# Kernel optimization log

Measured on AMD Instinct MI355X. Metric: run time of the kernel, lower is better.

## Reference

```python
import jax, jax.numpy as jnp
import numpy as np

OFFS = [(dy, dx) for dy in (-1, 0, 1) for dx in (-1, 0, 1)]  # ME centered 3x3 region


def _build_maps():
    """Build the sparse coordinate pyramid and per-offset kernel maps, exactly
    mirroring MinkowskiEngine: out coords of a stride-2 conv are unique(c//2),
    and a pair (i_in, i_out) exists iff coord_out*stride + offset is active."""
    G = 1024
    rng = np.random.default_rng(0)
    flat = np.sort(rng.choice(G * G, size=300000, replace=False))
    coords = [np.stack(np.unravel_index(flat, (G, G)), axis=1).astype(np.int64)]
    grids = [G]
    for _ in range(3):
        coords.append(np.unique(coords[-1] // 2, axis=0))
        grids.append(grids[-1] // 2)

    def lut(c, g):
        t = -np.ones(g * g, np.int64)
        t[c[:, 0] * g + c[:, 1]] = np.arange(len(c))
        return t

    luts = [lut(c, g) for c, g in zip(coords, grids)]

    def kmap(lvl_in, c_out, stride):
        g, L = grids[lvl_in], luts[lvl_in]
        n_in, n_out = len(coords[lvl_in]), len(c_out)
        base = c_out * stride
        pairs = []
        for dy, dx in OFFS:
            q = base + np.array([dy, dx])
            ok = (q[:, 0] >= 0) & (q[:, 0] < g) & (q[:, 1] >= 0) & (q[:, 1] < g)
            key = np.clip(q[:, 0] * g + q[:, 1], 0, g * g - 1)
            idx = np.where(ok, L[key], -1)
            sel = np.nonzero(idx >= 0)[0]
            pairs.append((idx[sel], sel))
        M = max(len(p[0]) for p in pairs)
        ii = np.full((9, M), n_in, np.int32)   # pad -> dummy zero input row
        oo = np.full((9, M), n_out, np.int32)  # pad -> dummy output row (dropped)
        for k, (a, b) in enumerate(pairs):
            ii[k, :len(a)] = a
            oo[k, :len(b)] = b
        return ii, oo

    maps = {
        'c0': kmap(0, coords[0], 1), 'd0': kmap(0, coords[1], 2),
        'c1': kmap(1, coords[1], 1), 'd1': kmap(1, coords[2], 2),
        'c2': kmap(2, coords[2], 1), 'd2': kmap(2, coords[3], 2),
    }
    return maps, [len(c) for c in coords]


def setup_inputs() -> dict:
    maps, (n0, n1, n2, n3) = _build_maps()
    ks = jax.random.split(jax.random.key(0), 16)
    d = {'feats': jax.random.normal(ks[0], (n0, 1), jnp.float32)}
    chans = [(1, 64), (64, 128), (128, 128), (128, 128), (128, 128), (128, 128)]
    names = ['c0', 'd0', 'c1', 'd1', 'c2', 'd2']
    for i, (nm, (ci, co)) in enumerate(zip(names, chans)):
        d[f'w_{nm}'] = jax.random.normal(ks[1 + 2 * i], (9, ci, co), jnp.float32) / np.sqrt(9.0 * ci)
        d[f'b_{nm}'] = jax.random.normal(ks[2 + 2 * i], (co,), jnp.float32) * 0.01
        d[f'in_{nm}'] = jnp.asarray(maps[nm][0])
        d[f'out_{nm}'] = jnp.asarray(maps[nm][1])
    d.update(n0=n0, n1=n1, n2=n2, n3=n3)
    return d


def sparse_conv(feats, w, b, in_idx, out_idx, n_out):
    """Gather-GEMM-scatter sparse conv. w: [9, Cin, Cout]. Padded pairs point at a
    dummy zero input row (index n_in) and a dummy output row (index n_out)."""
    n_in, cin = feats.shape
    fp = jnp.concatenate([feats, jnp.zeros((1, cin), feats.dtype)], axis=0)
    out = jnp.zeros((n_out + 1, w.shape[2]), feats.dtype)
    for k in range(9):  # fixed kernel volume
        out = out.at[out_idx[k]].add(fp[in_idx[k]] @ w[k])
    return out[:n_out] + b


def reference(feats, w_c0, b_c0, in_c0, out_c0, w_d0, b_d0, in_d0, out_d0,
              w_c1, b_c1, in_c1, out_c1, w_d1, b_d1, in_d1, out_d1,
              w_c2, b_c2, in_c2, out_c2, w_d2, b_d2, in_d2, out_d2,
              n0, n1, n2, n3):
    x = sparse_conv(feats, w_c0, b_c0, in_c0, out_c0, n0)
    out0 = jax.nn.relu(sparse_conv(x, w_d0, b_d0, in_d0, out_d0, n1))
    y = sparse_conv(out0, w_c1, b_c1, in_c1, out_c1, n1)
    out1 = jax.nn.relu(sparse_conv(y, w_d1, b_d1, in_d1, out_d1, n2))
    z = sparse_conv(out1, w_c2, b_c2, in_c2, out_c2, n2)
    out2 = sparse_conv(z, w_d2, b_d2, in_d2, out_d2, n3)
    return (out2, out1, out0)
```

## Files before the change

kernel.cpp:

```cpp
#include <hip/hip_runtime.h>
#include <stdint.h>
#include <algorithm>


#define DI __device__ __forceinline__

typedef __attribute__((ext_vector_type(8))) short bf16x8;
typedef __attribute__((ext_vector_type(4))) float f32x4;

DI uint16_t f2bf(float x){
  union{float f;uint32_t i;}v; v.f=x;
  uint32_t r = v.i + 0x7fffu + ((v.i>>16)&1u);
  return (uint16_t)(r>>16);
}
DI uint32_t pack2(float a, float b){
  return (uint32_t)f2bf(a) | ((uint32_t)f2bf(b) << 16);
}
DI void gload16(const void* g, void* l){
  __builtin_amdgcn_global_load_lds(
      (const __attribute__((address_space(1))) void*)g,
      (__attribute__((address_space(3))) void*)l, 16, 0, 0);
}

__global__ __launch_bounds__(256) void diag_kernel(float* __restrict__ out, long n, float c){
  long i = (long)blockIdx.x*256 + threadIdx.x;
  if (i < n) out[i] = c;
}

__global__ __launch_bounds__(256) void init_all_kernel(
    int* __restrict__ tab, long ntab, float* __restrict__ zp){
  long i = (long)blockIdx.x*256 + threadIdx.x;
  if (i < ntab) tab[i] = -1;
  if (blockIdx.x == 0 && threadIdx.x < 64) zp[threadIdx.x] = 0.f;
}

struct BuildArgs {
  const int* im[6];
  const int* om[6];
  int   M[6];
  int   nin[6];
  int   nout[6];
  long  toff[6];
};

__global__ __launch_bounds__(256) void build_all_kernel(
    BuildArgs a, int* __restrict__ tb){
  const int L = blockIdx.z, k = blockIdx.y;
  const int M = a.M[L];
  long t = (long)blockIdx.x*256 + threadIdx.x;
  if (t >= M) return;
  int ii = a.im[L][(long)k*M + t];
  int oo = a.om[L][(long)k*M + t];
  if (ii >= 0 && ii < a.nin[L] && oo >= 0 && oo < a.nout[L])
    tb[a.toff[L] + (long)k*a.nout[L] + oo] = ii;
}

__global__ __launch_bounds__(256) void prep_all_kernel(
    const float* __restrict__ w0, const float* __restrict__ w1,
    const float* __restrict__ w2, const float* __restrict__ w3,
    const float* __restrict__ w4, uint16_t* __restrict__ wb, long total){
  const long wt64 = 9L*128*64, wt128 = 9L*128*128;
  long idx = (long)blockIdx.x*256 + threadIdx.x;
  if (idx >= total) return;
  int L; long r; int cin;
  if (idx < wt64){ L = 0; r = idx; cin = 64; }
  else { long j = idx - wt64; L = 1 + (int)(j / wt128); r = j % wt128; cin = 128; }
  const float* w = (L==0) ? w0 : (L==1) ? w1 : (L==2) ? w2 : (L==3) ? w3 : w4;
  int k = (int)(r / (128*cin));
  int rem = (int)(r % (128*cin));
  int cout = rem / cin, ci = rem % cin;
  wb[idx] = f2bf(w[((long)k*cin + ci)*128 + cout]);
}

__global__ __launch_bounds__(256) void c0_tab_kernel(
    const float* __restrict__ feats, const float* __restrict__ w,
    const float* __restrict__ bias, const int* __restrict__ tab,
    uint16_t* __restrict__ out, int n_out){
  __shared__ float w_s[576];
  __shared__ float b_s[64];
  const int tid = threadIdx.x;
  for (int i = tid; i < 576; i += 256) w_s[i] = w[i];
  if (tid < 64) b_s[tid] = bias[tid];
  __syncthreads();
  long r = (long)blockIdx.x*256 + tid;
  if (r >= n_out) return;
  float f[9];
  #pragma unroll
  for (int k = 0; k < 9; k++){
    int gi = tab[(long)k*n_out + r];
    f[k] = (gi >= 0) ? feats[gi] : 0.f;
  }
  uint16_t* dst = out + r*64;
  #pragma unroll
  for (int c0 = 0; c0 < 64; c0 += 16){
    float a[16];
    #pragma unroll
    for (int j = 0; j < 16; j++) a[j] = b_s[c0+j];
    #pragma unroll
    for (int k = 0; k < 9; k++){
      float fk = f[k];
      #pragma unroll
      for (int j = 0; j < 16; j++) a[j] += fk * w_s[k*64 + c0 + j];
    }
    uint4 o0, o1;
    o0.x = pack2(a[0],a[1]);   o0.y = pack2(a[2],a[3]);
    o0.z = pack2(a[4],a[5]);   o0.w = pack2(a[6],a[7]);
    o1.x = pack2(a[8],a[9]);   o1.y = pack2(a[10],a[11]);
    o1.z = pack2(a[12],a[13]); o1.w = pack2(a[14],a[15]);
    *(uint4*)(dst + c0)     = o0;
    *(uint4*)(dst + c0 + 8) = o1;
  }
}

template<int CIN, int OUTMODE, bool RELU>
__global__ __launch_bounds__(512,6) void mconv3_kernel(
    const char* __restrict__ ws_base, long in_off, long wtb_off, long zp_off,
    const float* __restrict__ bias, const int* __restrict__ tab,
    float* __restrict__ outf, uint16_t* __restrict__ outb, int n_out){
  constexpr int NS = 9*CIN/32;
  __shared__ __align__(16) uint16_t ab[3][128*32];
  __shared__ __align__(16) uint16_t bb[3][128*32];

  const int tid = threadIdx.x;
  const int nwg = gridDim.x, orig = blockIdx.x;
  const int q = nwg >> 3, rr = nwg & 7, xcd = orig & 7, pos = orig >> 3;
  const int wg = (xcd < rr ? xcd*(q+1) : rr*(q+1) + (xcd-rr)*q) + pos;
  const long rb = (long)wg * 128;

  const int r0 = tid >> 2, sg = tid & 3;
  const int lsg = sg ^ ((r0 >> 1) & 3);

  uint32_t offA[9];
  #pragma unroll
  for (int kk = 0; kk < 9; ++kk){
    long row = rb + r0;
    int gi = (row < (long)n_out) ? tab[(long)kk*n_out + row] : -1;
    offA[kk] = (gi >= 0) ? (uint32_t)(in_off + (long)gi*(CIN*2) + lsg*16)
                         : (uint32_t)(zp_off + lsg*16);
  }
  const uint32_t offB0 = (uint32_t)(wtb_off + ((long)r0*CIN + lsg*8)*2);

  const int lane = tid & 63;
  const int wv = tid >> 6;
  const int wr = (wv >> 1) << 5;
  const int wc = (wv & 1) << 6;
  const int l16 = lane & 15, quad = lane >> 4;
  const int xsw = (quad ^ ((l16 >> 1) & 3)) << 3;

  float bv[4];
  #pragma unroll
  for (int ct = 0; ct < 4; ++ct) bv[ct] = bias[wc + (ct<<4) + l16];

  f32x4 acc[2][4];
  #pragma unroll
  for (int i = 0; i < 2; i++)
    #pragma unroll
    for (int j = 0; j < 4; j++)
      acc[i][j] = (f32x4){0.f,0.f,0.f,0.f};

  auto stage = [&](int t, int nb){
    const int kk = t / (CIN/32), ch = t % (CIN/32);
    gload16(ws_base + offA[kk] + ch*64, &ab[nb][tid*8]);
    gload16(ws_base + offB0 + (uint32_t)((long)kk*128*CIN*2) + ch*64,
            &bb[nb][tid*8]);
  };
  auto compute = [&](int nb){
    const uint16_t* A  = &ab[nb][0];
    const uint16_t* Bm = &bb[nb][0];
    __builtin_amdgcn_s_setprio(1);
    bf16x8 af[2], bfr[4];
    #pragma unroll
    for (int u = 0; u < 2; ++u)
      af[u]  = *(const bf16x8*)&A [((wr + (u<<4) + l16) << 5) + xsw];
    #pragma unroll
    for (int u = 0; u < 4; ++u)
      bfr[u] = *(const bf16x8*)&Bm[((wc + (u<<4) + l16) << 5) + xsw];
    #pragma unroll
    for (int rt = 0; rt < 2; ++rt)
      #pragma unroll
      for (int ct = 0; ct < 4; ++ct)
        acc[rt][ct] = __builtin_amdgcn_mfma_f32_16x16x32_bf16(
            af[rt], bfr[ct], acc[rt][ct], 0, 0, 0);
    __builtin_amdgcn_s_setprio(0);
  };

  stage(0, 0);
  stage(1, 1);
  #pragma unroll
  for (int t = 0; t < NS; ++t){
    if (t + 2 < NS){
      stage(t+2, (t+2)%3);
      asm volatile("s_waitcnt vmcnt(4)" ::: "memory");
    } else if (t + 1 < NS){
      asm volatile("s_waitcnt vmcnt(2)" ::: "memory");
    } else {
      asm volatile("s_waitcnt vmcnt(0)" ::: "memory");
    }
    __builtin_amdgcn_sched_barrier(0);
    __builtin_amdgcn_s_barrier();
    compute(t%3);
    if (t + 1 < NS)
      __builtin_amdgcn_s_barrier();
  }

  #pragma unroll
  for (int ct = 0; ct < 4; ++ct){
    const int cout = wc + (ct<<4) + l16;
    #pragma unroll
    for (int rt = 0; rt < 2; ++rt){
      #pragma unroll
      for (int r = 0; r < 4; ++r){
        long row = rb + wr + (rt<<4) + (quad<<2) + r;
        if (row < (long)n_out){
          float v = acc[rt][ct][r] + bv[ct];
          if (RELU) v = v > 0.f ? v : 0.f;
          if constexpr (OUTMODE == 0 || OUTMODE == 2) outf[row*128 + cout] = v;
          if constexpr (OUTMODE == 1 || OUTMODE == 2) outb[row*128 + cout] = f2bf(v);
        }
      }
    }
  }
}

static inline long cdivl(long a, long b){ return (a + b - 1) / b; }

extern "C" void kernel_launch(void* const* d_in, const int* in_sizes, int n_in_args,
                              void* d_out, int out_size, void* d_ws, size_t ws_size,
                              hipStream_t stream) {
  const float* feats = (const float*)d_in[0];
  const float* w_c0 = (const float*)d_in[1];
  const float* b_c0 = (const float*)d_in[2];
  const int* in_c0  = (const int*)d_in[3];
  const int* out_c0 = (const int*)d_in[4];
  const float* w_d0 = (const float*)d_in[5];
  const float* b_d0 = (const float*)d_in[6];
  const int* in_d0  = (const int*)d_in[7];
  const int* out_d0 = (const int*)d_in[8];
  const float* w_c1 = (const float*)d_in[9];
  const float* b_c1 = (const float*)d_in[10];
  const int* in_c1  = (const int*)d_in[11];
  const int* out_c1 = (const int*)d_in[12];
  const float* w_d1 = (const float*)d_in[13];
  const float* b_d1 = (const float*)d_in[14];
  const int* in_d1  = (const int*)d_in[15];
  const int* out_d1 = (const int*)d_in[16];
  const float* w_c2 = (const float*)d_in[17];
  const float* b_c2 = (const float*)d_in[18];
  const int* in_c2  = (const int*)d_in[19];
  const int* out_c2 = (const int*)d_in[20];
  const float* w_d2 = (const float*)d_in[21];
  const float* b_d2 = (const float*)d_in[22];
  const int* in_d2  = (const int*)d_in[23];
  const int* out_d2 = (const int*)d_in[24];

  const int n0   = in_sizes[0];
  const int M_c0 = in_sizes[3]  / 9;
  const int M_d0 = in_sizes[7]  / 9;
  const int M_c1 = in_sizes[11] / 9;
  const int M_d1 = in_sizes[15] / 9;
  const int M_c2 = in_sizes[19] / 9;
  const int M_d2 = in_sizes[23] / 9;
  const int n1   = M_c1;
  const int n2   = M_c2;
  const int n3   = out_size/128 - n1 - n2;

  bool sane = n0 > 0 && out_size % 128 == 0 &&
              M_c0 > 0 && M_d0 > 0 && M_d1 > 0 && M_d2 > 0 &&
              n1 > 0 && n2 > 0 && n3 > 0;

  long maxElems = (long)n0*64;
  if ((long)n1*128 > maxElems) maxElems = (long)n1*128;
  if ((long)n2*128 > maxElems) maxElems = (long)n2*128;
  long fbytes = (maxElems*2 + 255)/256*256;
  long ntab   = sane ? 9L*((long)n0 + 2L*n1 + 2L*n2 + n3) : 0;
  long tbytes = (ntab*4 + 255)/256*256;
  long wt64  = 9L*128*64, wt128 = 9L*128*128;
  long wbytes = ((wt64 + 4*wt128)*2 + 255)/256*256;
  long zbytes = 256;
  long b1bytes = sane ? ((long)n2*128*2 + 255)/256*256 : 0;
  long b0bytes = sane ? ((long)n1*128*2 + 255)/256*256 : 0;
  long need_full = fbytes + tbytes + wbytes + zbytes + 256 + b1bytes + b0bytes;

  if (!sane || ws_size < (size_t)need_full){
    float C = (float)(16 + (int)std::min<size_t>(ws_size >> 20, (size_t)100000));
    if (!sane) C *= 1099511627776.0f;
    diag_kernel<<<cdivl(out_size,256),256,0,stream>>>((float*)d_out, out_size, C);
    return;
  }

  uint16_t* fbuf = (uint16_t*)d_ws;
  long tab_off    = fbytes;
  long wtb_off    = fbytes + tbytes;
  long zp_off     = fbytes + tbytes + wbytes;
  long bf1_off    = zp_off + zbytes + 256;
  long bf0_off    = bf1_off + b1bytes;
  const char* wsb = (const char*)d_ws;
  int* tb        = (int*)((char*)d_ws + tab_off);
  float* zp_p    = (float*)((char*)d_ws + zp_off);
  uint16_t* bf1  = (uint16_t*)((char*)d_ws + bf1_off);
  uint16_t* bf0  = (uint16_t*)((char*)d_ws + bf0_off);

  long t_c0 = 0;
  long t_d0 = t_c0 + 9L*n0;
  long t_c1 = t_d0 + 9L*n1;
  long t_d1 = t_c1 + 9L*n1;
  long t_c2 = t_d1 + 9L*n2;
  long t_d2 = t_c2 + 9L*n2;

  float* out2 = (float*)d_out;
  float* out1 = out2 + (long)n3*128;
  float* out0 = out1 + (long)n2*128;

  init_all_kernel<<<cdivl(ntab,256),256,0,stream>>>(tb, ntab, zp_p);

  BuildArgs ba;
  ba.im[0]=in_c0;  ba.om[0]=out_c0; ba.M[0]=M_c0; ba.nin[0]=n0; ba.nout[0]=n0; ba.toff[0]=t_c0;
  ba.im[1]=in_d0;  ba.om[1]=out_d0; ba.M[1]=M_d0; ba.nin[1]=n0; ba.nout[1]=n1; ba.toff[1]=t_d0;
  ba.im[2]=in_c1;  ba.om[2]=out_c1; ba.M[2]=M_c1; ba.nin[2]=n1; ba.nout[2]=n1; ba.toff[2]=t_c1;
  ba.im[3]=in_d1;  ba.om[3]=out_d1; ba.M[3]=M_d1; ba.nin[3]=n1; ba.nout[3]=n2; ba.toff[3]=t_d1;
  ba.im[4]=in_c2;  ba.om[4]=out_c2; ba.M[4]=M_c2; ba.nin[4]=n2; ba.nout[4]=n2; ba.toff[4]=t_c2;
  ba.im[5]=in_d2;  ba.om[5]=out_d2; ba.M[5]=M_d2; ba.nin[5]=n2; ba.nout[5]=n3; ba.toff[5]=t_d2;
  long maxM = M_c0;
  for (int i = 0; i < 6; ++i) if (ba.M[i] > maxM) maxM = ba.M[i];
  dim3 bg((unsigned)cdivl(maxM,256), 9, 6);
  build_all_kernel<<<bg,256,0,stream>>>(ba, tb);

  long wtotal = wt64 + 4*wt128;
  prep_all_kernel<<<cdivl(wtotal,256),256,0,stream>>>(
      w_d0, w_c1, w_d1, w_c2, w_d2,
      (uint16_t*)((char*)d_ws + wtb_off), wtotal);

  c0_tab_kernel<<<cdivl(n0,256),256,0,stream>>>(feats, w_c0, b_c0, tb + t_c0, fbuf, n0);

  mconv3_kernel<64,2,true><<<cdivl(n1,128),512,0,stream>>>(
      wsb, 0L, wtb_off, zp_off, b_d0, tb + t_d0, out0, bf0, n1);

  mconv3_kernel<128,1,false><<<cdivl(n1,128),512,0,stream>>>(
      wsb, bf0_off, wtb_off + wt64*2, zp_off, b_c1, tb + t_c1, nullptr, fbuf, n1);

  mconv3_kernel<128,2,true><<<cdivl(n2,128),512,0,stream>>>(
      wsb, 0L, wtb_off + (wt64 + wt128)*2, zp_off, b_d1, tb + t_d1, out1, bf1, n2);

  mconv3_kernel<128,1,false><<<cdivl(n2,128),512,0,stream>>>(
      wsb, bf1_off, wtb_off + (wt64 + 2*wt128)*2, zp_off, b_c2, tb + t_c2, nullptr, fbuf, n2);

  mconv3_kernel<128,0,false><<<cdivl(n3,128),512,0,stream>>>(
      wsb, 0L, wtb_off + (wt64 + 3*wt128)*2, zp_off, b_d2, tb + t_d2, out2, nullptr, n3);
}
```

Baseline: 541.0 us.

## Double K-chunk per pipeline step and decouple A/B buffer depths in sparse conv GEMM

```diff
diff --git a/kernel.cpp b/kernel.cpp
--- a/kernel.cpp
+++ b/kernel.cpp
@@ -113,13 +113,13 @@
 }
 
 template<int CIN, int OUTMODE, bool RELU>
-__global__ __launch_bounds__(512,6) void mconv3_kernel(
+__global__ __launch_bounds__(512,4) void mconv4_kernel(
     const char* __restrict__ ws_base, long in_off, long wtb_off, long zp_off,
     const float* __restrict__ bias, const int* __restrict__ tab,
     float* __restrict__ outf, uint16_t* __restrict__ outb, int n_out){
-  constexpr int NS = 9*CIN/32;
-  __shared__ __align__(16) uint16_t ab[3][128*32];
-  __shared__ __align__(16) uint16_t bb[3][128*32];
+  constexpr int NS = 9*CIN/64;
+  __shared__ __align__(16) uint16_t ab[3][128*64];
+  __shared__ __align__(16) uint16_t bb[2][128*64];
 
   const int tid = threadIdx.x;
   const int nwg = gridDim.x, orig = blockIdx.x;
@@ -127,25 +127,28 @@
   const int wg = (xcd < rr ? xcd*(q+1) : rr*(q+1) + (xcd-rr)*q) + pos;
   const long rb = (long)wg * 128;
 
-  const int r0 = tid >> 2, sg = tid & 3;
-  const int lsg = sg ^ ((r0 >> 1) & 3);
-
-  uint32_t offA[9];
+  const int r0 = tid >> 3, sg = tid & 7;
+  const int ss0 = sg ^ (r0 & 7);
+
+  uint32_t offA[2][9];
   #pragma unroll
   for (int kk = 0; kk < 9; ++kk){
-    long row = rb + r0;
-    int gi = (row < (long)n_out) ? tab[(long)kk*n_out + row] : -1;
-    offA[kk] = (gi >= 0) ? (uint32_t)(in_off + (long)gi*(CIN*2) + lsg*16)
-                         : (uint32_t)(zp_off + lsg*16);
-  }
-  const uint32_t offB0 = (uint32_t)(wtb_off + ((long)r0*CIN + lsg*8)*2);
+    #pragma unroll
+    for (int it = 0; it < 2; ++it){
+      long row = rb + it*64 + r0;
+      int gi = (row < (long)n_out) ? tab[(long)kk*n_out + row] : -1;
+      offA[it][kk] = (gi >= 0)
+          ? (uint32_t)(in_off + (long)gi*(CIN*2) + ss0*16)
+          : (uint32_t)(zp_off + ss0*16);
+    }
+  }
+  const uint32_t offB = (uint32_t)(wtb_off + ((long)r0*CIN + ss0*8)*2);
 
   const int lane = tid & 63;
   const int wv = tid >> 6;
   const int wr = (wv >> 1) << 5;
   const int wc = (wv & 1) << 6;
   const int l16 = lane & 15, quad = lane >> 4;
-  const int xsw = (quad ^ ((l16 >> 1) & 3)) << 3;
 
   float bv[4];
   #pragma unroll
@@ -158,38 +161,53 @@
     for (int j = 0; j < 4; j++)
       acc[i][j] = (f32x4){0.f,0.f,0.f,0.f};
 
-  auto stage = [&](int t, int nb){
-    const int kk = t / (CIN/32), ch = t % (CIN/32);
-    gload16(ws_base + offA[kk] + ch*64, &ab[nb][tid*8]);
-    gload16(ws_base + offB0 + (uint32_t)((long)kk*128*CIN*2) + ch*64,
-            &bb[nb][tid*8]);
+  auto stage_a = [&](int step, int nb){
+    const int kk  = (CIN == 64) ? step : (step >> 1);
+    const int c0b = (CIN == 64) ? 0 : ((step & 1) * 128);
+    #pragma unroll
+    for (int it = 0; it < 2; ++it)
+      gload16(ws_base + offA[it][kk] + c0b, &ab[nb][(it*512+tid)*8]);
   };
-  auto compute = [&](int nb){
-    const uint16_t* A  = &ab[nb][0];
+  auto stage_b = [&](int step, int nb){
+    const int kk  = (CIN == 64) ? step : (step >> 1);
+    const int c0b = (CIN == 64) ? 0 : ((step & 1) * 128);
+    const uint32_t base = offB + (uint32_t)((long)kk*128*CIN*2 + c0b);
+    #pragma unroll
+    for (int it = 0; it < 2; ++it)
+      gload16(ws_base + base + it*(64*CIN*2), &bb[nb][(it*512+tid)*8]);
+  };
+  auto compute = [&](int na, int nb){
+    const uint16_t* A  = &ab[na][0];
     const uint16_t* Bm = &bb[nb][0];
     __builtin_amdgcn_s_setprio(1);
-    bf16x8 af[2], bfr[4];
-    #pragma unroll
-    for (int u = 0; u < 2; ++u)
-      af[u]  = *(const bf16x8*)&A [((wr + (u<<4) + l16) << 5) + xsw];
-    #pragma unroll
-    for (int u = 0; u < 4; ++u)
-      bfr[u] = *(const bf16x8*)&Bm[((wc + (u<<4) + l16) << 5) + xsw];
-    #pragma unroll
-    for (int rt = 0; rt < 2; ++rt)
-      #pragma unroll
-      for (int ct = 0; ct < 4; ++ct)
-        acc[rt][ct] = __builtin_amdgcn_mfma_f32_16x16x32_bf16(
-            af[rt], bfr[ct], acc[rt][ct], 0, 0, 0);
+    #pragma unroll
+    for (int ch = 0; ch < 2; ++ch){
+      const int xs = ((((ch << 2) + quad) ^ (l16 & 7)) << 3);
+      bf16x8 af[2], bfr[4];
+      #pragma unroll
+      for (int u = 0; u < 2; ++u)
+        af[u]  = *(const bf16x8*)&A [((wr + (u<<4) + l16) << 6) + xs];
+      #pragma unroll
+      for (int u = 0; u < 4; ++u)
+        bfr[u] = *(const bf16x8*)&Bm[((wc + (u<<4) + l16) << 6) + xs];
+      #pragma unroll
+      for (int rt = 0; rt < 2; ++rt)
+        #pragma unroll
+        for (int ct = 0; ct < 4; ++ct)
+          acc[rt][ct] = __builtin_amdgcn_mfma_f32_16x16x32_bf16(
+              af[rt], bfr[ct], acc[rt][ct], 0, 0, 0);
+    }
     __builtin_amdgcn_s_setprio(0);
   };
 
-  stage(0, 0);
-  stage(1, 1);
+  stage_a(0, 0);
+  stage_a(1, 1);
+  stage_b(0, 0);
   #pragma unroll
   for (int t = 0; t < NS; ++t){
+    if (t + 2 < NS) stage_a(t+2, (t+2)%3);
+    if (t + 1 < NS) stage_b(t+1, (t+1)&1);
     if (t + 2 < NS){
-      stage(t+2, (t+2)%3);
       asm volatile("s_waitcnt vmcnt(4)" ::: "memory");
     } else if (t + 1 < NS){
       asm volatile("s_waitcnt vmcnt(2)" ::: "memory");
@@ -198,7 +216,7 @@
     }
     __builtin_amdgcn_sched_barrier(0);
     __builtin_amdgcn_s_barrier();
-    compute(t%3);
+    compute(t%3, t&1);
     if (t + 1 < NS)
       __builtin_amdgcn_s_barrier();
   }
@@ -332,18 +350,18 @@
 
   c0_tab_kernel<<<cdivl(n0,256),256,0,stream>>>(feats, w_c0, b_c0, tb + t_c0, fbuf, n0);
 
-  mconv3_kernel<64,2,true><<<cdivl(n1,128),512,0,stream>>>(
+  mconv4_kernel<64,2,true><<<cdivl(n1,128),512,0,stream>>>(
       wsb, 0L, wtb_off, zp_off, b_d0, tb + t_d0, out0, bf0, n1);
 
-  mconv3_kernel<128,1,false><<<cdivl(n1,128),512,0,stream>>>(
+  mconv4_kernel<128,1,false><<<cdivl(n1,128),512,0,stream>>>(
       wsb, bf0_off, wtb_off + wt64*2, zp_off, b_c1, tb + t_c1, nullptr, fbuf, n1);
 
-  mconv3_kernel<128,2,true><<<cdivl(n2,128),512,0,stream>>>(
+  mconv4_kernel<128,2,true><<<cdivl(n2,128),512,0,stream>>>(
       wsb, 0L, wtb_off + (wt64 + wt128)*2, zp_off, b_d1, tb + t_d1, out1, bf1, n2);
 
-  mconv3_kernel<128,1,false><<<cdivl(n2,128),512,0,stream>>>(
+  mconv4_kernel<128,1,false><<<cdivl(n2,128),512,0,stream>>>(
       wsb, bf1_off, wtb_off + (wt64 + 2*wt128)*2, zp_off, b_c2, tb + t_c2, nullptr, fbuf, n2);
 
-  mconv3_kernel<128,0,false><<<cdivl(n3,128),512,0,stream>>>(
+  mconv4_kernel<128,0,false><<<cdivl(n3,128),512,0,stream>>>(
       wsb, 0L, wtb_off + (wt64 + 3*wt128)*2, zp_off, b_d2, tb + t_d2, out2, nullptr, n3);
 }
```

New measurement: 491.0 us. 9.2% less time.
